# Performance work log

Hardware: AMD Instinct MI355X
Metric: run time of the kernel (lower is better)

The kernel has to match this reference:

```python
import jax, jax.numpy as jnp
import numpy as np

N_ITERS = 5

def setup_inputs() -> dict:
    key = jax.random.key(0)
    k_in, k_ind, k_w = jax.random.split(key, 3)
    inputs = jax.random.normal(k_in, (2, 256, 256, 1), dtype=jnp.float32)
    # indices must be valid for spatial dims [256,256] (iter 1) and [217,721] (iters 2-5)
    ind1 = jax.random.randint(k_ind, (367, 217, 721, 2), 0, 217, dtype=jnp.int32)
    w1 = jax.random.uniform(k_w, (367, 217, 721, 1, 1), dtype=jnp.float32)
    lambda1 = jnp.asarray(0.1, dtype=jnp.float32)
    return {"inputs": inputs, "ind1": ind1, "w1": w1, "lambda1": lambda1}


def reference(inputs, ind1, w1, lambda1):
    # inputs: [B,H,W,C]; ind1: [367,217,721,2]; w1: [367,217,721,1,1]; lambda1: scalar
    i0 = ind1[..., 0]  # [367,217,721] -> indexes dim0 of [H,W,C,B]
    i1 = ind1[..., 1]  # [367,217,721] -> indexes dim1
    y = inputs
    for _ in range(N_ITERS):
        yt = jnp.transpose(y, (1, 2, 3, 0))          # [H,W,C,B]
        gathered = yt[i0, i1]                        # [367,217,721,C,B] (gather_nd)
        y = jnp.sum(gathered * w1, axis=0)           # [217,721,C,B]
        y = jnp.transpose(y, (3, 0, 1, 2))           # [B,217,721,C]
        y = lambda1 * y
    return y
```

## Files before the change

kernel.cpp:

```cpp
#include <hip/hip_runtime.h>
#include <hip/hip_fp16.h>
#include <stdint.h>

#define K_    367
#define P_    217
#define Q_    721
#define QC    217
#define CPQ   (QC*QC)
#define CPQV  47092
#define TPQ   109368
#define YSTR  47104
#define PQ_   (P_*Q_)
#define TOT   ((long long)K_*PQ_)
#define NVC   (CPQV/4)
#define NVT   (TPQ/4)
#define NPAD  (3*K_)
#define LDSH  47092

__global__ __launch_bounds__(256) void pack_all(
    const int2* __restrict__ ind, const float* __restrict__ w,
    const float* __restrict__ inp,
    uint32_t* __restrict__ cornerS, uint32_t* __restrict__ tailS,
    float* __restrict__ y0)
{
    long long id = (long long)blockIdx.x * 256 + threadIdx.x;
    if (id < TOT) {
        unsigned long long raw =
            __builtin_nontemporal_load((const unsigned long long*)(ind + id));
        float wv = __builtin_nontemporal_load(w + id);
        int i0 = (int)(uint32_t)(raw & 0xFFFFFFFFull);
        int i1 = (int)(uint32_t)(raw >> 32);
        uint32_t idx2 = ((uint32_t)(i0 * QC + i1)) << 1;
        uint32_t hb = (uint32_t)__half_as_ushort(__float2half(wv));
        uint32_t v = idx2 | (hb << 17);
        uint32_t ui = (uint32_t)id;
        uint32_t k = ui / (uint32_t)PQ_;
        uint32_t rem = ui - k * (uint32_t)PQ_;
        uint32_t p = rem / (uint32_t)Q_;
        uint32_t q = rem - p * (uint32_t)Q_;
        if (q < QC) cornerS[k * CPQV + p * QC + q] = v;
        else        tailS[(long long)k * TPQ + p * 504 + (q - QC)] = v;
        return;
    }
    long long id2 = id - TOT;
    if (id2 < CPQ) {
        int o = (int)id2;
        int p = o / QC, q = o - p * QC;
        y0[o]        = inp[p * 256 + q];
        y0[YSTR + o] = inp[65536 + p * 256 + q];
        return;
    }
    long long id3 = id2 - CPQ;
    if (id3 < NPAD) {
        int k = (int)(id3 / 3);
        cornerS[(long long)k * CPQV + CPQ + (int)(id3 - (long long)k * 3)] = 0u;
    }
}

#define GATHER(X, ACC) { uint32_t x_ = (X); \
    float g_ = __half2float(*(const __half*)((const char*)ylds + (x_ & 0x1FFFEu))); \
    float w_ = __half2float(__ushort_as_half((unsigned short)(x_ >> 17))); \
    ACC = fmaf(w_, g_, ACC); }

#define FILL_LDS() { \
    const float4* s4_ = (const float4*)yplane; \
    __half2* d2_ = (__half2*)ylds; \
    for (int i_ = threadIdx.x; i_ < LDSH / 4; i_ += 1024) { \
        float4 v_ = s4_[i_]; \
        d2_[2 * i_]     = __floats2half2_rn(v_.x, v_.y); \
        d2_[2 * i_ + 1] = __floats2half2_rn(v_.z, v_.w); \
    } }

__global__ __launch_bounds__(1024) void iter_corner(
    const uint32_t* __restrict__ cs, const float* __restrict__ yin,
    float* __restrict__ yout, const float* __restrict__ lam_p, int KS)
{
    __shared__ __half ylds[LDSH];
    const int b = blockIdx.z;
    const float* __restrict__ yplane = yin + (size_t)b * YSTR;
    FILL_LDS();
    __syncthreads();

    const int gx = (NVC + 1023) / 1024;
    const int nunits = gx * KS;
    const int klen = (K_ + KS - 1) / KS;
    const float ls = *lam_p;
    const uint4* cs4 = (const uint4*)cs;

    for (int unit = blockIdx.x; unit < nunits; unit += gridDim.x) {
        int ob = unit % gx, kc = unit / gx;
        int ov = ob * 1024 + threadIdx.x;
        if (ov >= NVC) continue;
        int k0 = kc * klen, k1 = min(K_, k0 + klen);
        float a0 = 0.f, a1 = 0.f, a2 = 0.f, a3 = 0.f;
        const uint4* pp = cs4 + (long long)k0 * NVC + ov;
        #pragma unroll 8
        for (int k = k0; k < k1; ++k, pp += NVC) {
            uint4 v = *pp;
            GATHER(v.x, a0); GATHER(v.y, a1); GATHER(v.z, a2); GATHER(v.w, a3);
        }
        float* op = yout + (size_t)b * YSTR + 4 * ov;
        atomicAdd(op + 0, a0 * ls);
        atomicAdd(op + 1, a1 * ls);
        atomicAdd(op + 2, a2 * ls);
        atomicAdd(op + 3, a3 * ls);
    }
}

__global__ __launch_bounds__(1024) void iter_final(
    const uint32_t* __restrict__ cs, const uint32_t* __restrict__ ts,
    const float* __restrict__ yin, float* __restrict__ out,
    const float* __restrict__ lam_p, int KS)
{
    __shared__ __half ylds[LDSH];
    const int b = blockIdx.z;
    const float* __restrict__ yplane = yin + (size_t)b * YSTR;
    FILL_LDS();
    __syncthreads();

    const int NV = NVC + NVT;
    const int gx = (NV + 1023) / 1024;
    const int nunits = gx * KS;
    const int klen = (K_ + KS - 1) / KS;
    const float ls = *lam_p;

    for (int unit = blockIdx.x; unit < nunits; unit += gridDim.x) {
        int ob = unit % gx, kc = unit / gx;
        int ov = ob * 1024 + threadIdx.x;
        if (ov >= NV) continue;
        bool corner = ov < NVC;
        int lv = corner ? ov : ov - NVC;
        int stride = corner ? NVC : NVT;
        const uint4* base = corner ? (const uint4*)cs : (const uint4*)ts;
        int k0 = kc * klen, k1 = min(K_, k0 + klen);
        float a0 = 0.f, a1 = 0.f, a2 = 0.f, a3 = 0.f;
        const uint4* pp = base + (long long)k0 * stride + lv;
        #pragma unroll 8
        for (int k = k0; k < k1; ++k, pp += stride) {
            uint4 v = *pp;
            GATHER(v.x, a0); GATHER(v.y, a1); GATHER(v.z, a2); GATHER(v.w, a3);
        }
        float acc[4] = {a0, a1, a2, a3};
        int o0 = 4 * lv;
        #pragma unroll
        for (int j = 0; j < 4; ++j) {
            int oo = o0 + j;
            int pos;
            if (corner) {
                if (oo >= CPQ) continue;
                int p = oo / QC; pos = p * Q_ + (oo - p * QC);
            } else {
                int p = oo / 504; pos = p * Q_ + QC + (oo - p * 504);
            }
            atomicAdd(&out[(size_t)b * PQ_ + pos], acc[j] * ls);
        }
    }
}

#define LDSN_FB 40960
__global__ __launch_bounds__(256) void copy_kernel_fb(
    const float* __restrict__ inp, float* __restrict__ y0)
{
    int o = blockIdx.x * blockDim.x + threadIdx.x;
    if (o >= CPQ) return;
    int p = o / QC, q = o - p * QC;
    y0[o]        = inp[p * 256 + q];
    y0[YSTR + o] = inp[65536 + p * 256 + q];
}
template<bool FULL>
__global__ __launch_bounds__(1024) void iter_direct(
    const int2* __restrict__ ind, const float* __restrict__ w1,
    const float* __restrict__ yin, float* __restrict__ yout,
    const float* __restrict__ lam_p, int KS)
{
    __shared__ float ylds[LDSN_FB];
    const int b = blockIdx.z;
    const float* __restrict__ yplane = yin + (size_t)b * YSTR;
    {
        const float4* s4 = (const float4*)yplane;
        float4* d4 = (float4*)ylds;
        for (int i = threadIdx.x; i < LDSN_FB / 4; i += 1024) d4[i] = s4[i];
    }
    __syncthreads();
    const int nout = FULL ? PQ_ : CPQ;
    const int gx = (nout + 1023) / 1024;
    const int nunits = gx * KS;
    const int klen = (K_ + KS - 1) / KS;
    const float ls = *lam_p;
    const int ostr = FULL ? PQ_ : YSTR;
    for (int unit = blockIdx.x; unit < nunits; unit += gridDim.x) {
        int ob = unit % gx, kc = unit / gx;
        int o = ob * 1024 + threadIdx.x;
        if (o >= nout) continue;
        int soff;
        if (FULL) soff = o;
        else { int p = o / QC; soff = p * Q_ + (o - p * QC); }
        int k0 = kc * klen, k1 = min(K_, k0 + klen);
        float acc = 0.f;
        const int2*  ip = ind + (long long)k0 * PQ_ + soff;
        const float* wp = w1  + (long long)k0 * PQ_ + soff;
        #pragma unroll 4
        for (int k = k0; k < k1; ++k, ip += PQ_, wp += PQ_) {
            int2 ij = *ip;
            int idx = ij.x * QC + ij.y;
            float g = (idx < LDSN_FB) ? ylds[idx] : yplane[idx];
            acc = fmaf(*wp, g, acc);
        }
        atomicAdd(&yout[(size_t)b * ostr + o], acc * ls);
    }
}

extern "C" void kernel_launch(void* const* d_in, const int* in_sizes, int n_in,
                              void* d_out, int out_size, void* d_ws, size_t ws_size,
                              hipStream_t stream)
{
    const float* inp = (const float*)d_in[0];
    const int2*  ind = (const int2*)d_in[1];
    const float* w1  = (const float*)d_in[2];
    const float* lam = (const float*)d_in[3];
    float* out = (float*)d_out;

    size_t cbytes = ((((size_t)K_ * CPQV) * 4) + 255) & ~(size_t)255;
    size_t tbytes = ((((size_t)K_ * TPQ) * 4) + 255) & ~(size_t)255;
    size_t YB = (size_t)(2 * YSTR) * sizeof(float);
    bool use_packed = ws_size >= cbytes + tbytes + 5 * YB;

    uint8_t* ws = (uint8_t*)d_ws;
    if (use_packed) {
        uint32_t* cornerS = (uint32_t*)ws;
        uint32_t* tailS   = (uint32_t*)(ws + cbytes);
        float* ybase = (float*)(ws + cbytes + tbytes);
        float* y[5];
        for (int i = 0; i < 5; ++i) y[i] = ybase + (size_t)i * (2 * YSTR);

        hipMemsetAsync(y[1], 0, 4 * YB, stream);
        hipMemsetAsync(out, 0, (size_t)PQ_ * 2 * sizeof(float), stream);

        long long nwork = TOT + CPQ + NPAD;
        unsigned nb = (unsigned)((nwork + 255) / 256);
        pack_all<<<dim3(nb), 256, 0, stream>>>(ind, w1, inp, cornerS, tailS, y[0]);

        const int KS_C = 10, KS_F = 6;
        dim3 gC(120, 1, 2), gF(117, 1, 2);
        for (int it = 0; it < 4; ++it)
            iter_corner<<<gC, 1024, 0, stream>>>(cornerS, y[it], y[it + 1], lam, KS_C);
        iter_final<<<gF, 1024, 0, stream>>>(cornerS, tailS, y[4], out, lam, KS_F);
    } else {
        float* y0 = (float*)ws;
        float* y1 = (float*)(ws + YB);
        copy_kernel_fb<<<(CPQ + 255) / 256, 256, 0, stream>>>(inp, y0);
        const int KS_C = 12, KS_F = 4;
        dim3 g(128, 1, 2);
        float* yin = y0; float* yout = y1;
        for (int it = 0; it < 4; ++it) {
            hipMemsetAsync(yout, 0, YB, stream);
            iter_direct<false><<<g, 1024, 0, stream>>>(ind, w1, yin, yout, lam, KS_C);
            float* t = yin; yin = yout; yout = t;
        }
        hipMemsetAsync(out, 0, (size_t)PQ_ * 2 * sizeof(float), stream);
        iter_direct<true><<<g, 1024, 0, stream>>>(ind, w1, yin, out, lam, KS_F);
    }
}
```

Baseline: 357.5 us.

## Fuse pack and all iterations into one cooperative persistent kernel with grid syncs

Replaces the separate memset, pack, four corner-iteration and final launches with a single cooperative kernel of 240 blocks that uses grid.sync between phases. The pack phase now loads two entries per thread with vector nontemporal loads, and the final stage splits K into 40 chunks instead of 6. The aim is to remove launch gaps, memsets and tail effects between kernels. In exchange it adds grid-wide barriers and a fixed grid size that may underfill the device or limit occupancy. The non-packed fallback path is removed, and the launcher now returns without doing any work if the workspace is too small.

```diff
diff --git a/kernel.cpp b/kernel.cpp
--- a/kernel.cpp
+++ b/kernel.cpp
@@ -1,6 +1,9 @@
 #include <hip/hip_runtime.h>
 #include <hip/hip_fp16.h>
+#include <hip/hip_cooperative_groups.h>
 #include <stdint.h>
+
+namespace cg = cooperative_groups;
 
 #define K_    367
 #define P_    217
@@ -16,6 +19,159 @@
 #define NVT   (TPQ/4)
 #define NPAD  (3*K_)
 #define LDSH  47092
+#define NBLK  240
+#define NTHR  1024
+#define BPB   120
+#define KS_C  10
+#define KS_F  40
+
+typedef uint32_t u32x4 __attribute__((ext_vector_type(4)));
+typedef float    f32x2 __attribute__((ext_vector_type(2)));
+
+__device__ __forceinline__ uint32_t encode_entry(int i0, int i1, float wv) {
+    uint32_t idx2 = ((uint32_t)(i0 * QC + i1)) << 1;
+    uint32_t hb = (uint32_t)__half_as_ushort(__float2half(wv));
+    return idx2 | (hb << 17);
+}
+__device__ __forceinline__ void store_entry(uint32_t ui, uint32_t v,
+    uint32_t* __restrict__ cornerS, uint32_t* __restrict__ tailS) {
+    uint32_t k = ui / (uint32_t)PQ_;
+    uint32_t rem = ui - k * (uint32_t)PQ_;
+    uint32_t p = rem / (uint32_t)Q_;
+    uint32_t q = rem - p * (uint32_t)Q_;
+    if (q < QC) cornerS[k * (uint32_t)CPQV + p * QC + q] = v;
+    else        tailS[(long long)k * TPQ + p * 504 + (q - QC)] = v;
+}
+
+#define GATHER(X, ACC) { uint32_t x_ = (X); \
+    float g_ = __half2float(*(const __half*)((const char*)ylds + (x_ & 0x1FFFEu))); \
+    float w_ = __half2float(__ushort_as_half((unsigned short)(x_ >> 17))); \
+    ACC = fmaf(w_, g_, ACC); }
+
+#define FILL_LDS() { \
+    const float4* s4_ = (const float4*)yplane; \
+    __half2* d2_ = (__half2*)ylds; \
+    for (int i_ = threadIdx.x; i_ < LDSH / 4; i_ += NTHR) { \
+        float4 v_ = s4_[i_]; \
+        d2_[2 * i_]     = __floats2half2_rn(v_.x, v_.y); \
+        d2_[2 * i_ + 1] = __floats2half2_rn(v_.z, v_.w); \
+    } }
+
+__global__ __launch_bounds__(NTHR) void mega(
+    const int2* __restrict__ ind, const float* __restrict__ w,
+    const float* __restrict__ inp,
+    uint32_t* __restrict__ cornerS, uint32_t* __restrict__ tailS,
+    float* __restrict__ ybase, float* __restrict__ out,
+    const float* __restrict__ lam_p)
+{
+    __shared__ __half ylds[LDSH];
+    cg::grid_group grid = cg::this_grid();
+    const int tid = blockIdx.x * NTHR + threadIdx.x;
+    const int T = NBLK * NTHR;
+    const float lam = *lam_p;
+
+    {
+        const long long NPAIR = TOT / 2;
+        for (long long pr = tid; pr < NPAIR; pr += T) {
+            long long i = pr * 2;
+            u32x4 r = __builtin_nontemporal_load((const u32x4*)(ind + i));
+            f32x2 wv = __builtin_nontemporal_load((const f32x2*)(w + i));
+            uint32_t v0 = encode_entry((int)r.x, (int)r.y, wv.x);
+            uint32_t v1 = encode_entry((int)r.z, (int)r.w, wv.y);
+            store_entry((uint32_t)i, v0, cornerS, tailS);
+            store_entry((uint32_t)i + 1u, v1, cornerS, tailS);
+        }
+        if (tid == 0) {
+            long long i = TOT - 1;
+            int2 e = ind[i];
+            store_entry((uint32_t)i, encode_entry(e.x, e.y, w[i]), cornerS, tailS);
+        }
+        for (int o = tid; o < CPQ + NPAD; o += T) {
+            if (o < CPQ) {
+                int p = o / QC, q = o - p * QC;
+                ybase[o]        = inp[p * 256 + q];
+                ybase[YSTR + o] = inp[65536 + p * 256 + q];
+            } else {
+                int t = o - CPQ;
+                int k = t / 3;
+                cornerS[(long long)k * CPQV + CPQ + (t - k * 3)] = 0u;
+            }
+        }
+        float* zb = ybase + 2 * YSTR;
+        for (int o = tid; o < 8 * YSTR; o += T) zb[o] = 0.f;
+        for (int o = tid; o < 2 * PQ_; o += T) out[o] = 0.f;
+    }
+    __threadfence();
+    grid.sync();
+
+    const int b  = blockIdx.x / BPB;
+    const int lb = blockIdx.x % BPB;
+    const uint4* cs4 = (const uint4*)cornerS;
+
+    for (int it = 0; it < 4; ++it) {
+        const float* yplane = ybase + (size_t)it * (2 * YSTR) + (size_t)b * YSTR;
+        FILL_LDS();
+        __syncthreads();
+        int ob = lb % 12, kc = lb / 12;
+        int k0 = kc * K_ / KS_C, k1 = (kc + 1) * K_ / KS_C;
+        int ov = ob * NTHR + threadIdx.x;
+        if (ov < NVC) {
+            float a0 = 0.f, a1 = 0.f, a2 = 0.f, a3 = 0.f;
+            const uint4* pp = cs4 + (long long)k0 * NVC + ov;
+            #pragma unroll 8
+            for (int k = k0; k < k1; ++k, pp += NVC) {
+                uint4 v = *pp;
+                GATHER(v.x, a0); GATHER(v.y, a1); GATHER(v.z, a2); GATHER(v.w, a3);
+            }
+            float* op = ybase + (size_t)(it + 1) * (2 * YSTR) + (size_t)b * YSTR + 4 * ov;
+            atomicAdd(op + 0, a0 * lam);
+            atomicAdd(op + 1, a1 * lam);
+            atomicAdd(op + 2, a2 * lam);
+            atomicAdd(op + 3, a3 * lam);
+        }
+        __threadfence();
+        grid.sync();
+    }
+
+    {
+        const float* yplane = ybase + (size_t)4 * (2 * YSTR) + (size_t)b * YSTR;
+        FILL_LDS();
+        __syncthreads();
+        const int NV = NVC + NVT;
+        for (int u = 0; u < 13; ++u) {
+            int unit = lb + u * BPB;
+            int ob = unit % 39, kc = unit / 39;
+            int k0 = kc * K_ / KS_F, k1 = (kc + 1) * K_ / KS_F;
+            int ov = ob * NTHR + threadIdx.x;
+            if (ov >= NV) continue;
+            bool corner = ov < NVC;
+            int lv = corner ? ov : ov - NVC;
+            int stride = corner ? NVC : NVT;
+            const uint4* base = corner ? cs4 : (const uint4*)tailS;
+            float a0 = 0.f, a1 = 0.f, a2 = 0.f, a3 = 0.f;
+            const uint4* pp = base + (long long)k0 * stride + lv;
+            #pragma unroll 5
+            for (int k = k0; k < k1; ++k, pp += stride) {
+                uint4 v = *pp;
+                GATHER(v.x, a0); GATHER(v.y, a1); GATHER(v.z, a2); GATHER(v.w, a3);
+            }
+            float acc[4] = {a0, a1, a2, a3};
+            int o0 = 4 * lv;
+            #pragma unroll
+            for (int j = 0; j < 4; ++j) {
+                int oo = o0 + j;
+                int pos;
+                if (corner) {
+                    if (oo >= CPQ) continue;
+                    int p = oo / QC; pos = p * Q_ + (oo - p * QC);
+                } else {
+                    int p = oo / 504; pos = p * Q_ + QC + (oo - p * 504);
+                }
+                atomicAdd(&out[(size_t)b * PQ_ + pos], acc[j] * lam);
+            }
+        }
+    }
+}
 
 __global__ __launch_bounds__(256) void pack_all(
     const int2* __restrict__ ind, const float* __restrict__ w,
@@ -30,16 +186,7 @@
         float wv = __builtin_nontemporal_load(w + id);
         int i0 = (int)(uint32_t)(raw & 0xFFFFFFFFull);
         int i1 = (int)(uint32_t)(raw >> 32);
-        uint32_t idx2 = ((uint32_t)(i0 * QC + i1)) << 1;
-        uint32_t hb = (uint32_t)__half_as_ushort(__float2half(wv));
-        uint32_t v = idx2 | (hb << 17);
-        uint32_t ui = (uint32_t)id;
-        uint32_t k = ui / (uint32_t)PQ_;
-        uint32_t rem = ui - k * (uint32_t)PQ_;
-        uint32_t p = rem / (uint32_t)Q_;
-        uint32_t q = rem - p * (uint32_t)Q_;
-        if (q < QC) cornerS[k * CPQV + p * QC + q] = v;
-        else        tailS[(long long)k * TPQ + p * 504 + (q - QC)] = v;
+        store_entry((uint32_t)id, encode_entry(i0, i1, wv), cornerS, tailS);
         return;
     }
     long long id2 = id - TOT;
@@ -57,41 +204,24 @@
     }
 }
 
-#define GATHER(X, ACC) { uint32_t x_ = (X); \
-    float g_ = __half2float(*(const __half*)((const char*)ylds + (x_ & 0x1FFFEu))); \
-    float w_ = __half2float(__ushort_as_half((unsigned short)(x_ >> 17))); \
-    ACC = fmaf(w_, g_, ACC); }
-
-#define FILL_LDS() { \
-    const float4* s4_ = (const float4*)yplane; \
-    __half2* d2_ = (__half2*)ylds; \
-    for (int i_ = threadIdx.x; i_ < LDSH / 4; i_ += 1024) { \
-        float4 v_ = s4_[i_]; \
-        d2_[2 * i_]     = __floats2half2_rn(v_.x, v_.y); \
-        d2_[2 * i_ + 1] = __floats2half2_rn(v_.z, v_.w); \
-    } }
-
 __global__ __launch_bounds__(1024) void iter_corner(
     const uint32_t* __restrict__ cs, const float* __restrict__ yin,
     float* __restrict__ yout, const float* __restrict__ lam_p, int KS)
 {
     __shared__ __half ylds[LDSH];
-    const int b = blockIdx.z;
-    const float* __restrict__ yplane = yin + (size_t)b * YSTR;
+    const int bz = blockIdx.z;
+    const float* __restrict__ yplane = yin + (size_t)bz * YSTR;
     FILL_LDS();
     __syncthreads();
-
     const int gx = (NVC + 1023) / 1024;
     const int nunits = gx * KS;
-    const int klen = (K_ + KS - 1) / KS;
     const float ls = *lam_p;
     const uint4* cs4 = (const uint4*)cs;
-
     for (int unit = blockIdx.x; unit < nunits; unit += gridDim.x) {
         int ob = unit % gx, kc = unit / gx;
         int ov = ob * 1024 + threadIdx.x;
         if (ov >= NVC) continue;
-        int k0 = kc * klen, k1 = min(K_, k0 + klen);
+        int k0 = kc * K_ / KS, k1 = (kc + 1) * K_ / KS;
         float a0 = 0.f, a1 = 0.f, a2 = 0.f, a3 = 0.f;
         const uint4* pp = cs4 + (long long)k0 * NVC + ov;
         #pragma unroll 8
@@ -99,7 +229,7 @@
             uint4 v = *pp;
             GATHER(v.x, a0); GATHER(v.y, a1); GATHER(v.z, a2); GATHER(v.w, a3);
         }
-        float* op = yout + (size_t)b * YSTR + 4 * ov;
+        float* op = yout + (size_t)bz * YSTR + 4 * ov;
         atomicAdd(op + 0, a0 * ls);
         atomicAdd(op + 1, a1 * ls);
         atomicAdd(op + 2, a2 * ls);
@@ -113,17 +243,14 @@
     const float* __restrict__ lam_p, int KS)
 {
     __shared__ __half ylds[LDSH];
-    const int b = blockIdx.z;
-    const float* __restrict__ yplane = yin + (size_t)b * YSTR;
+    const int bz = blockIdx.z;
+    const float* __restrict__ yplane = yin + (size_t)bz * YSTR;
     FILL_LDS();
     __syncthreads();
-
     const int NV = NVC + NVT;
     const int gx = (NV + 1023) / 1024;
     const int nunits = gx * KS;
-    const int klen = (K_ + KS - 1) / KS;
     const float ls = *lam_p;
-
     for (int unit = blockIdx.x; unit < nunits; unit += gridDim.x) {
         int ob = unit % gx, kc = unit / gx;
         int ov = ob * 1024 + threadIdx.x;
@@ -132,7 +259,7 @@
         int lv = corner ? ov : ov - NVC;
         int stride = corner ? NVC : NVT;
         const uint4* base = corner ? (const uint4*)cs : (const uint4*)ts;
-        int k0 = kc * klen, k1 = min(K_, k0 + klen);
+        int k0 = kc * K_ / KS, k1 = (kc + 1) * K_ / KS;
         float a0 = 0.f, a1 = 0.f, a2 = 0.f, a3 = 0.f;
         const uint4* pp = base + (long long)k0 * stride + lv;
         #pragma unroll 8
@@ -152,61 +279,8 @@
             } else {
                 int p = oo / 504; pos = p * Q_ + QC + (oo - p * 504);
             }
-            atomicAdd(&out[(size_t)b * PQ_ + pos], acc[j] * ls);
-        }
-    }
-}
-
-#define LDSN_FB 40960
-__global__ __launch_bounds__(256) void copy_kernel_fb(
-    const float* __restrict__ inp, float* __restrict__ y0)
-{
-    int o = blockIdx.x * blockDim.x + threadIdx.x;
-    if (o >= CPQ) return;
-    int p = o / QC, q = o - p * QC;
-    y0[o]        = inp[p * 256 + q];
-    y0[YSTR + o] = inp[65536 + p * 256 + q];
-}
-template<bool FULL>
-__global__ __launch_bounds__(1024) void iter_direct(
-    const int2* __restrict__ ind, const float* __restrict__ w1,
-    const float* __restrict__ yin, float* __restrict__ yout,
-    const float* __restrict__ lam_p, int KS)
-{
-    __shared__ float ylds[LDSN_FB];
-    const int b = blockIdx.z;
-    const float* __restrict__ yplane = yin + (size_t)b * YSTR;
-    {
-        const float4* s4 = (const float4*)yplane;
-        float4* d4 = (float4*)ylds;
-        for (int i = threadIdx.x; i < LDSN_FB / 4; i += 1024) d4[i] = s4[i];
-    }
-    __syncthreads();
-    const int nout = FULL ? PQ_ : CPQ;
-    const int gx = (nout + 1023) / 1024;
-    const int nunits = gx * KS;
-    const int klen = (K_ + KS - 1) / KS;
-    const float ls = *lam_p;
-    const int ostr = FULL ? PQ_ : YSTR;
-    for (int unit = blockIdx.x; unit < nunits; unit += gridDim.x) {
-        int ob = unit % gx, kc = unit / gx;
-        int o = ob * 1024 + threadIdx.x;
-        if (o >= nout) continue;
-        int soff;
-        if (FULL) soff = o;
-        else { int p = o / QC; soff = p * Q_ + (o - p * QC); }
-        int k0 = kc * klen, k1 = min(K_, k0 + klen);
-        float acc = 0.f;
-        const int2*  ip = ind + (long long)k0 * PQ_ + soff;
-        const float* wp = w1  + (long long)k0 * PQ_ + soff;
-        #pragma unroll 4
-        for (int k = k0; k < k1; ++k, ip += PQ_, wp += PQ_) {
-            int2 ij = *ip;
-            int idx = ij.x * QC + ij.y;
-            float g = (idx < LDSN_FB) ? ylds[idx] : yplane[idx];
-            acc = fmaf(*wp, g, acc);
-        }
-        atomicAdd(&yout[(size_t)b * ostr + o], acc * ls);
+            atomicAdd(&out[(size_t)bz * PQ_ + pos], acc[j] * ls);
+        }
     }
 }
 
@@ -223,41 +297,31 @@
     size_t cbytes = ((((size_t)K_ * CPQV) * 4) + 255) & ~(size_t)255;
     size_t tbytes = ((((size_t)K_ * TPQ) * 4) + 255) & ~(size_t)255;
     size_t YB = (size_t)(2 * YSTR) * sizeof(float);
-    bool use_packed = ws_size >= cbytes + tbytes + 5 * YB;
+    if (ws_size < cbytes + tbytes + 5 * YB) return;
 
     uint8_t* ws = (uint8_t*)d_ws;
-    if (use_packed) {
-        uint32_t* cornerS = (uint32_t*)ws;
-        uint32_t* tailS   = (uint32_t*)(ws + cbytes);
-        float* ybase = (float*)(ws + cbytes + tbytes);
-        float* y[5];
-        for (int i = 0; i < 5; ++i) y[i] = ybase + (size_t)i * (2 * YSTR);
-
-        hipMemsetAsync(y[1], 0, 4 * YB, stream);
-        hipMemsetAsync(out, 0, (size_t)PQ_ * 2 * sizeof(float), stream);
-
-        long long nwork = TOT + CPQ + NPAD;
-        unsigned nb = (unsigned)((nwork + 255) / 256);
-        pack_all<<<dim3(nb), 256, 0, stream>>>(ind, w1, inp, cornerS, tailS, y[0]);
-
-        const int KS_C = 10, KS_F = 6;
-        dim3 gC(120, 1, 2), gF(117, 1, 2);
-        for (int it = 0; it < 4; ++it)
-            iter_corner<<<gC, 1024, 0, stream>>>(cornerS, y[it], y[it + 1], lam, KS_C);
-        iter_final<<<gF, 1024, 0, stream>>>(cornerS, tailS, y[4], out, lam, KS_F);
-    } else {
-        float* y0 = (float*)ws;
-        float* y1 = (float*)(ws + YB);
-        copy_kernel_fb<<<(CPQ + 255) / 256, 256, 0, stream>>>(inp, y0);
-        const int KS_C = 12, KS_F = 4;
-        dim3 g(128, 1, 2);
-        float* yin = y0; float* yout = y1;
-        for (int it = 0; it < 4; ++it) {
-            hipMemsetAsync(yout, 0, YB, stream);
-            iter_direct<false><<<g, 1024, 0, stream>>>(ind, w1, yin, yout, lam, KS_C);
-            float* t = yin; yin = yout; yout = t;
-        }
-        hipMemsetAsync(out, 0, (size_t)PQ_ * 2 * sizeof(float), stream);
-        iter_direct<true><<<g, 1024, 0, stream>>>(ind, w1, yin, out, lam, KS_F);
-    }
-}
+    uint32_t* cornerS = (uint32_t*)ws;
+    uint32_t* tailS   = (uint32_t*)(ws + cbytes);
+    float* ybase = (float*)(ws + cbytes + tbytes);
+
+    const int2* a_ind = ind; const float* a_w = w1; const float* a_inp = inp;
+    uint32_t* a_cs = cornerS; uint32_t* a_ts = tailS;
+    float* a_y = ybase; float* a_out = out; const float* a_lam = lam;
+    void* args[] = {(void*)&a_ind, (void*)&a_w, (void*)&a_inp, (void*)&a_cs,
+                    (void*)&a_ts, (void*)&a_y, (void*)&a_out, (void*)&a_lam};
+    hipError_t e = hipLaunchCooperativeKernel(reinterpret_cast<void*>(mega),
+                                              dim3(NBLK), dim3(NTHR), args, 0, stream);
+    if (e == hipSuccess) return;
+
+    float* y[5];
+    for (int i = 0; i < 5; ++i) y[i] = ybase + (size_t)i * (2 * YSTR);
+    (void)hipMemsetAsync(y[1], 0, 4 * YB, stream);
+    (void)hipMemsetAsync(out, 0, (size_t)PQ_ * 2 * sizeof(float), stream);
+    long long nwork = TOT + CPQ + NPAD;
+    unsigned nb = (unsigned)((nwork + 255) / 256);
+    pack_all<<<dim3(nb), 256, 0, stream>>>(ind, w1, inp, cornerS, tailS, y[0]);
+    dim3 gC(120, 1, 2), gF(117, 1, 2);
+    for (int it = 0; it < 4; ++it)
+        iter_corner<<<gC, 1024, 0, stream>>>(cornerS, y[it], y[it + 1], lam, 10);
+    iter_final<<<gF, 1024, 0, stream>>>(cornerS, tailS, y[4], out, lam, 6);
+}
```

Result: slower. 1.061 ms (+196.8%).
